# Performance work log

Hardware: AMD Instinct MI355X
Metric: run time of the kernel (lower is better)

## Reference

```python
import jax, jax.numpy as jnp
import numpy as np

THRESH = 0.3
EPS = 1e-8
M = 256
D = 768


def setup_inputs() -> dict:
    key = jax.random.key(0)
    kx, kb, ka, kn = jax.random.split(key, 4)
    x = jax.random.normal(kx, (1, D), dtype=jnp.float32)
    base = jax.random.normal(kb, (M, D), dtype=jnp.float32)
    # correlate memories with x so that a realistic fraction passes the 0.3 cosine threshold
    alpha = jax.random.uniform(ka, (M,), minval=0.0, maxval=0.8)
    mem = alpha[:, None] * x[0][None, :] + jnp.sqrt(1.0 - alpha**2)[:, None] * base
    # pre-sampled injection noise (original: torch.randn * 0.1 per W element)
    noise = 0.1 * jax.random.normal(kn, (M, M, D), dtype=jnp.float32)
    return {"x": x, "mem": mem, "noise": noise}


def reference(x, mem, noise):
    # x: [1, D] query embedding; mem: [M, D] memory bank (k == memory embeddings)
    d = x.shape[-1]
    xv = x[0]                                   # [D]
    nx = jnp.maximum(jnp.linalg.norm(xv), EPS)
    nm = jnp.linalg.norm(mem, axis=-1)          # [M]
    nm_s = jnp.maximum(nm, EPS)
    Sx = xv.sum()
    Sm = mem.sum(-1)                            # [M]

    kx_dot = mem @ xv                           # [M] dot(k_i, x)
    mx_cos = kx_dot / (nm_s * nx)               # [M] cos(x, m_j) == cos(k_i, x)
    mask = (mx_cos > THRESH).astype(x.dtype)    # active memories A
    cnt = mask.sum()

    km_dot = mem @ mem.T                        # [M, M] dot(k_i, m_j)
    km_cos = km_dot / (nm_s[:, None] * nm_s[None, :])

    # c[a, i] = cos(k_i, m_a) + cos(k_i, x)  (scalar added to all D dims of k_i)
    c = km_cos.T + mx_cos[None, :]              # [M, M]

    # ||k'_{a,i}||^2 = ||k_i||^2 + 2 c sum(k_i) + D c^2
    nkp = jnp.sqrt(jnp.maximum(nm[None, :]**2 + 2.0 * c * Sm[None, :] + d * c**2, EPS**2))

    # cos(k'_{a,i}, x) = (dot(k_i,x) + c*sum(x)) / (||k'|| * ||x||)
    cos_kp_x = (kx_dot[None, :] + c * Sx) / (nkp * nx)

    # mean over a' in A of cos(k'_{a,i}, m_{a'}) in closed form
    A1 = (km_dot * (mask / nm_s)[None, :]).sum(-1)   # [M] (i-indexed)
    A2 = ((mask * Sm) / nm_s).sum()                  # scalar
    denom = nkp * jnp.maximum(cnt, 1.0)
    mean_cos_km = jnp.where(cnt > 0, (A1[None, :] + c * A2) / denom, 0.0)

    # W_{a,i} = k'_{a,i} + mean sim to x + mean sim to active mems; then noise; O_prev = 0
    W = mem[None, :, :] + (c + cos_kp_x + mean_cos_km)[:, :, None]   # [M, M, D]
    out = (W + noise) * mask[:, None, None]     # zero rows for inactive memories
    return out
```

## Files before the change

kernel.cpp:

```cpp
#include <hip/hip_runtime.h>
#include <hip/hip_bf16.h>
#include <math.h>

#define M 256
#define D 768
#define D4 (D/4)
#define THRESH 0.3
#define EPS 1e-8

typedef float vfloat4 __attribute__((ext_vector_type(4)));

#define WS_SM    0
#define WS_NM2   256
#define WS_KX    512
#define WS_MASK  768
#define WS_SX    1024
#define WS_NX2   1025
#define WS_MEMT  2048
#define WS_ST    (2048 + D * M)

__global__ __launch_bounds__(256) void k1_stats_transpose(const float* __restrict__ x,
                                                          const float* __restrict__ mem,
                                                          float* __restrict__ ws) {
    const int r = blockIdx.x;
    const int t = threadIdx.x;
    const float* row = (r < M) ? (mem + (size_t)r * D) : x;

    double s = 0.0, sq = 0.0, dt = 0.0;
    for (int d = t; d < D; d += 256) {
        float mf = row[d];
        double m = (double)mf;
        double xv = (double)x[d];
        s += m; sq += m * m; dt += m * xv;
        if (r < M) ws[WS_MEMT + (d >> 2) * (M * 4) + r * 4 + (d & 3)] = mf;
    }
    __shared__ double sh0[256], sh1[256], sh2[256];
    sh0[t] = s; sh1[t] = sq; sh2[t] = dt;
    __syncthreads();
    for (int k = 128; k > 0; k >>= 1) {
        if (t < k) { sh0[t] += sh0[t + k]; sh1[t] += sh1[t + k]; sh2[t] += sh2[t + k]; }
        __syncthreads();
    }
    if (t == 0) {
        if (r < M) {
            ws[WS_SM + r]  = (float)sh0[0];
            ws[WS_NM2 + r] = (float)sh1[0];
            ws[WS_KX + r]  = (float)sh2[0];
        } else {
            ws[WS_SX]  = (float)sh0[0];
            ws[WS_NX2] = (float)sh1[0];
        }
    }
}

__global__ __launch_bounds__(256) void k3_s(const float* __restrict__ mem,
                                            float* __restrict__ ws) {
    const int i = blockIdx.x;
    const int a = threadIdx.x;

    const double nxd   = fmax(sqrt(fmax((double)ws[WS_NX2], 0.0)), EPS);
    const double nm2ad = (double)ws[WS_NM2 + a];
    const double nmsad = fmax(sqrt(fmax(nm2ad, 0.0)), EPS);
    const double mxad  = (double)ws[WS_KX + a] / (nmsad * nxd);
    const float maska = (mxad > THRESH) ? 1.0f : 0.0f;
    const float nmsa  = (float)nmsad;
    if (i == 0) ws[WS_MASK + a] = maska;

    __shared__ vfloat4 lrow4[D4];
    if (a < D4) lrow4[a] = ((const vfloat4*)mem)[(size_t)i * D4 + a];
    __syncthreads();

    const vfloat4* memT4 = (const vfloat4*)(ws + WS_MEMT);
    float acc0 = 0.f, acc1 = 0.f, acc2 = 0.f, acc3 = 0.f;
    for (int dq = 0; dq < D4; dq += 4) {
        vfloat4 v0 = memT4[(dq + 0) * M + a]; vfloat4 l0 = lrow4[dq + 0];
        vfloat4 v1 = memT4[(dq + 1) * M + a]; vfloat4 l1 = lrow4[dq + 1];
        vfloat4 v2 = memT4[(dq + 2) * M + a]; vfloat4 l2 = lrow4[dq + 2];
        vfloat4 v3 = memT4[(dq + 3) * M + a]; vfloat4 l3 = lrow4[dq + 3];
        acc0 += v0.x * l0.x + v0.y * l0.y + v0.z * l0.z + v0.w * l0.w;
        acc1 += v1.x * l1.x + v1.y * l1.y + v1.z * l1.z + v1.w * l1.w;
        acc2 += v2.x * l2.x + v2.y * l2.y + v2.z * l2.z + v2.w * l2.w;
        acc3 += v3.x * l3.x + v3.y * l3.y + v3.z * l3.z + v3.w * l3.w;
    }
    const float g = (acc0 + acc1) + (acc2 + acc3);

    __shared__ float shc[M], sha[M], shr[M];
    shc[a] = maska;
    sha[a] = maska * ws[WS_SM + a] / nmsa;
    shr[a] = (maska / nmsa) * g;
    __syncthreads();
    for (int k = 128; k > 0; k >>= 1) {
        if (a < k) { shc[a] += shc[a + k]; sha[a] += sha[a + k]; shr[a] += shr[a + k]; }
        __syncthreads();
    }
    const float cnt = shc[0];
    const float A2  = sha[0];
    const float A1  = shr[0];

    const float nm2i = ws[WS_NM2 + i];
    const float Smi  = ws[WS_SM + i];
    const float kxi  = ws[WS_KX + i];
    const float nmsi = fmaxf(sqrtf(fmaxf(nm2i, 0.f)), 1e-8f);
    const float nx   = (float)nxd;
    const float Sx   = ws[WS_SX];
    const float mxi  = kxi / (nmsi * nx);

    const float c = g / (nmsa * nmsi) + mxi;
    const float nkp = sqrtf(fmaxf(nm2i + 2.f * c * Smi + (float)D * c * c, 1e-16f));
    const float cos_kp_x = (kxi + c * Sx) / (nkp * nx);
    const float mean_cos_km = (cnt > 0.f) ? (A1 + c * A2) / (nkp * fmaxf(cnt, 1.f)) : 0.f;

    ws[WS_ST + i * M + a] = c + cos_kp_x + mean_cos_km;
}

__global__ __launch_bounds__(D4) void k4_final(const float* __restrict__ mem,
                                               const float* __restrict__ noise,
                                               const float* __restrict__ ws,
                                               float* __restrict__ out) {
    const int a = blockIdx.y;
    const int i0 = blockIdx.x * 16;
    const int t  = threadIdx.x;

    vfloat4* out4 = (vfloat4*)out;
    const size_t base = ((size_t)a * M + i0) * D4 + t;

    if (ws[WS_MASK + a] == 0.0f) {
        const vfloat4 z = (vfloat4){0.f, 0.f, 0.f, 0.f};
        #pragma unroll
        for (int il = 0; il < 16; ++il)
            __builtin_nontemporal_store(z, out4 + base + (size_t)il * D4);
        return;
    }

    const vfloat4* mem4   = (const vfloat4*)mem;
    const vfloat4* noise4 = (const vfloat4*)noise;

    __shared__ float ssh[16];
    if (t < 16) ssh[t] = ws[WS_ST + (i0 + t) * M + a];
    __syncthreads();

    #pragma unroll 4
    for (int il = 0; il < 16; ++il) {
        const float s = ssh[il];
        vfloat4 m = mem4[(size_t)(i0 + il) * D4 + t];
        vfloat4 n = __builtin_nontemporal_load(noise4 + base + (size_t)il * D4);
        vfloat4 o;
        o.x = m.x + s + n.x;
        o.y = m.y + s + n.y;
        o.z = m.z + s + n.z;
        o.w = m.w + s + n.w;
        __builtin_nontemporal_store(o, out4 + base + (size_t)il * D4);
    }
}

extern "C" void kernel_launch(void* const* d_in, const int* in_sizes, int n_in,
                              void* d_out, int out_size, void* d_ws, size_t ws_size,
                              hipStream_t stream) {
    const float* x     = (const float*)d_in[0];
    const float* mem   = (const float*)d_in[1];
    const float* noise = (const float*)d_in[2];
    float* out = (float*)d_out;
    float* ws  = (float*)d_ws;

    k1_stats_transpose<<<dim3(M + 1), dim3(256), 0, stream>>>(x, mem, ws);
    k3_s<<<dim3(M), dim3(256), 0, stream>>>(mem, ws);
    k4_final<<<dim3(16, M), dim3(D4), 0, stream>>>(mem, noise, ws, out);
}
```

Baseline: 339.3 us.

## Fuse three kernels into one cooperative kernel with grid-wide syncs

Replaces the stats/transpose, score and output kernels with a single cooperative launch of 512 blocks that uses grid.sync between phases. The final phase is remapped so each 256-thread block streams 8 groups of 16 rows, with fully unrolled vector loads and stores. The aim is to remove the extra launch gaps and get more in-flight memory traffic in the large noise-to-output stream. In exchange, the work now depends on co-residency of 512 blocks and pays grid-barrier cost, and the big streaming phase runs on a fixed small grid instead of 4096 blocks.

```diff
diff --git a/kernel.cpp b/kernel.cpp
--- a/kernel.cpp
+++ b/kernel.cpp
@@ -1,12 +1,15 @@
 #include <hip/hip_runtime.h>
-#include <hip/hip_bf16.h>
+#include <hip/hip_cooperative_groups.h>
 #include <math.h>
+
+namespace cg = cooperative_groups;
 
 #define M 256
 #define D 768
 #define D4 (D/4)
 #define THRESH 0.3
 #define EPS 1e-8
+#define NBLK 512
 
 typedef float vfloat4 __attribute__((ext_vector_type(4)));
 
@@ -19,137 +22,152 @@
 #define WS_MEMT  2048
 #define WS_ST    (2048 + D * M)
 
-__global__ __launch_bounds__(256) void k1_stats_transpose(const float* __restrict__ x,
-                                                          const float* __restrict__ mem,
-                                                          float* __restrict__ ws) {
-    const int r = blockIdx.x;
+__global__ __launch_bounds__(256, 2) void fused(const float* __restrict__ x,
+                                                const float* __restrict__ mem,
+                                                const float* __restrict__ noise,
+                                                float* __restrict__ ws,
+                                                float* __restrict__ out) {
+    const int b = blockIdx.x;
     const int t = threadIdx.x;
-    const float* row = (r < M) ? (mem + (size_t)r * D) : x;
+    cg::grid_group grid = cg::this_grid();
 
-    double s = 0.0, sq = 0.0, dt = 0.0;
-    for (int d = t; d < D; d += 256) {
-        float mf = row[d];
-        double m = (double)mf;
-        double xv = (double)x[d];
-        s += m; sq += m * m; dt += m * xv;
-        if (r < M) ws[WS_MEMT + (d >> 2) * (M * 4) + r * 4 + (d & 3)] = mf;
-    }
     __shared__ double sh0[256], sh1[256], sh2[256];
-    sh0[t] = s; sh1[t] = sq; sh2[t] = dt;
-    __syncthreads();
-    for (int k = 128; k > 0; k >>= 1) {
-        if (t < k) { sh0[t] += sh0[t + k]; sh1[t] += sh1[t + k]; sh2[t] += sh2[t + k]; }
+    __shared__ vfloat4 lrow4[D4];
+    __shared__ float shc[M], sha[M], shr[M];
+    __shared__ float ssh[8][16];
+    __shared__ float shm[8];
+
+    if (b <= M) {
+        const float* row = (b < M) ? (mem + (size_t)b * D) : x;
+        double s = 0.0, sq = 0.0, dt = 0.0;
+        for (int d = t; d < D; d += 256) {
+            float mf = row[d];
+            double m = (double)mf;
+            double xv = (double)x[d];
+            s += m; sq += m * m; dt += m * xv;
+            if (b < M) ws[WS_MEMT + (d >> 2) * (M * 4) + b * 4 + (d & 3)] = mf;
+        }
+        sh0[t] = s; sh1[t] = sq; sh2[t] = dt;
         __syncthreads();
-    }
-    if (t == 0) {
-        if (r < M) {
-            ws[WS_SM + r]  = (float)sh0[0];
-            ws[WS_NM2 + r] = (float)sh1[0];
-            ws[WS_KX + r]  = (float)sh2[0];
-        } else {
-            ws[WS_SX]  = (float)sh0[0];
-            ws[WS_NX2] = (float)sh1[0];
+        for (int k = 128; k > 0; k >>= 1) {
+            if (t < k) { sh0[t] += sh0[t + k]; sh1[t] += sh1[t + k]; sh2[t] += sh2[t + k]; }
+            __syncthreads();
+        }
+        if (t == 0) {
+            if (b < M) {
+                ws[WS_SM + b]  = (float)sh0[0];
+                ws[WS_NM2 + b] = (float)sh1[0];
+                ws[WS_KX + b]  = (float)sh2[0];
+            } else {
+                ws[WS_SX]  = (float)sh0[0];
+                ws[WS_NX2] = (float)sh1[0];
+            }
         }
     }
-}
+    grid.sync();
 
-__global__ __launch_bounds__(256) void k3_s(const float* __restrict__ mem,
-                                            float* __restrict__ ws) {
-    const int i = blockIdx.x;
-    const int a = threadIdx.x;
+    if (b < M) {
+        const int i = b;
+        const int a = t;
 
-    const double nxd   = fmax(sqrt(fmax((double)ws[WS_NX2], 0.0)), EPS);
-    const double nm2ad = (double)ws[WS_NM2 + a];
-    const double nmsad = fmax(sqrt(fmax(nm2ad, 0.0)), EPS);
-    const double mxad  = (double)ws[WS_KX + a] / (nmsad * nxd);
-    const float maska = (mxad > THRESH) ? 1.0f : 0.0f;
-    const float nmsa  = (float)nmsad;
-    if (i == 0) ws[WS_MASK + a] = maska;
+        const double nxd   = fmax(sqrt(fmax((double)ws[WS_NX2], 0.0)), EPS);
+        const double nm2ad = (double)ws[WS_NM2 + a];
+        const double nmsad = fmax(sqrt(fmax(nm2ad, 0.0)), EPS);
+        const double mxad  = (double)ws[WS_KX + a] / (nmsad * nxd);
+        const float maska = (mxad > THRESH) ? 1.0f : 0.0f;
+        const float nmsa  = (float)nmsad;
+        if (i == 0) ws[WS_MASK + a] = maska;
 
-    __shared__ vfloat4 lrow4[D4];
-    if (a < D4) lrow4[a] = ((const vfloat4*)mem)[(size_t)i * D4 + a];
-    __syncthreads();
+        if (a < D4) lrow4[a] = ((const vfloat4*)mem)[(size_t)i * D4 + a];
+        __syncthreads();
 
-    const vfloat4* memT4 = (const vfloat4*)(ws + WS_MEMT);
-    float acc0 = 0.f, acc1 = 0.f, acc2 = 0.f, acc3 = 0.f;
-    for (int dq = 0; dq < D4; dq += 4) {
-        vfloat4 v0 = memT4[(dq + 0) * M + a]; vfloat4 l0 = lrow4[dq + 0];
-        vfloat4 v1 = memT4[(dq + 1) * M + a]; vfloat4 l1 = lrow4[dq + 1];
-        vfloat4 v2 = memT4[(dq + 2) * M + a]; vfloat4 l2 = lrow4[dq + 2];
-        vfloat4 v3 = memT4[(dq + 3) * M + a]; vfloat4 l3 = lrow4[dq + 3];
-        acc0 += v0.x * l0.x + v0.y * l0.y + v0.z * l0.z + v0.w * l0.w;
-        acc1 += v1.x * l1.x + v1.y * l1.y + v1.z * l1.z + v1.w * l1.w;
-        acc2 += v2.x * l2.x + v2.y * l2.y + v2.z * l2.z + v2.w * l2.w;
-        acc3 += v3.x * l3.x + v3.y * l3.y + v3.z * l3.z + v3.w * l3.w;
+        const vfloat4* memT4 = (const vfloat4*)(ws + WS_MEMT);
+        float acc0 = 0.f, acc1 = 0.f, acc2 = 0.f, acc3 = 0.f;
+        for (int dq = 0; dq < D4; dq += 4) {
+            vfloat4 v0 = memT4[(dq + 0) * M + a]; vfloat4 l0 = lrow4[dq + 0];
+            vfloat4 v1 = memT4[(dq + 1) * M + a]; vfloat4 l1 = lrow4[dq + 1];
+            vfloat4 v2 = memT4[(dq + 2) * M + a]; vfloat4 l2 = lrow4[dq + 2];
+            vfloat4 v3 = memT4[(dq + 3) * M + a]; vfloat4 l3 = lrow4[dq + 3];
+            acc0 += v0.x * l0.x + v0.y * l0.y + v0.z * l0.z + v0.w * l0.w;
+            acc1 += v1.x * l1.x + v1.y * l1.y + v1.z * l1.z + v1.w * l1.w;
+            acc2 += v2.x * l2.x + v2.y * l2.y + v2.z * l2.z + v2.w * l2.w;
+            acc3 += v3.x * l3.x + v3.y * l3.y + v3.z * l3.z + v3.w * l3.w;
+        }
+        const float g = (acc0 + acc1) + (acc2 + acc3);
+
+        shc[a] = maska;
+        sha[a] = maska * ws[WS_SM + a] / nmsa;
+        shr[a] = (maska / nmsa) * g;
+        __syncthreads();
+        for (int k = 128; k > 0; k >>= 1) {
+            if (a < k) { shc[a] += shc[a + k]; sha[a] += sha[a + k]; shr[a] += shr[a + k]; }
+            __syncthreads();
+        }
+        const float cnt = shc[0];
+        const float A2  = sha[0];
+        const float A1  = shr[0];
+
+        const float nm2i = ws[WS_NM2 + i];
+        const float Smi  = ws[WS_SM + i];
+        const float kxi  = ws[WS_KX + i];
+        const float nmsi = fmaxf(sqrtf(fmaxf(nm2i, 0.f)), 1e-8f);
+        const float nx   = (float)nxd;
+        const float Sx   = ws[WS_SX];
+        const float mxi  = kxi / (nmsi * nx);
+
+        const float c = g / (nmsa * nmsi) + mxi;
+        const float nkp = sqrtf(fmaxf(nm2i + 2.f * c * Smi + (float)D * c * c, 1e-16f));
+        const float cos_kp_x = (kxi + c * Sx) / (nkp * nx);
+        const float mean_cos_km = (cnt > 0.f) ? (A1 + c * A2) / (nkp * fmaxf(cnt, 1.f)) : 0.f;
+
+        ws[WS_ST + i * M + a] = c + cos_kp_x + mean_cos_km;
     }
-    const float g = (acc0 + acc1) + (acc2 + acc3);
+    grid.sync();
 
-    __shared__ float shc[M], sha[M], shr[M];
-    shc[a] = maska;
-    sha[a] = maska * ws[WS_SM + a] / nmsa;
-    shr[a] = (maska / nmsa) * g;
-    __syncthreads();
-    for (int k = 128; k > 0; k >>= 1) {
-        if (a < k) { shc[a] += shc[a + k]; sha[a] += sha[a + k]; shr[a] += shr[a + k]; }
+    {
+        const int u0 = b * 8;
+        if (t < 128) {
+            const int j  = t >> 4;
+            const int il = t & 15;
+            const int u  = u0 + j;
+            const int a  = u >> 4;
+            const int i0 = (u & 15) << 4;
+            ssh[j][il] = ws[WS_ST + (i0 + il) * M + a];
+        }
+        if (t < 8) shm[t] = ws[WS_MASK + ((u0 + t) >> 4)];
         __syncthreads();
-    }
-    const float cnt = shc[0];
-    const float A2  = sha[0];
-    const float A1  = shr[0];
 
-    const float nm2i = ws[WS_NM2 + i];
-    const float Smi  = ws[WS_SM + i];
-    const float kxi  = ws[WS_KX + i];
-    const float nmsi = fmaxf(sqrtf(fmaxf(nm2i, 0.f)), 1e-8f);
-    const float nx   = (float)nxd;
-    const float Sx   = ws[WS_SX];
-    const float mxi  = kxi / (nmsi * nx);
+        vfloat4* out4         = (vfloat4*)out;
+        const vfloat4* noise4 = (const vfloat4*)noise;
+        const vfloat4* mem4   = (const vfloat4*)mem;
 
-    const float c = g / (nmsa * nmsi) + mxi;
-    const float nkp = sqrtf(fmaxf(nm2i + 2.f * c * Smi + (float)D * c * c, 1e-16f));
-    const float cos_kp_x = (kxi + c * Sx) / (nkp * nx);
-    const float mean_cos_km = (cnt > 0.f) ? (A1 + c * A2) / (nkp * fmaxf(cnt, 1.f)) : 0.f;
-
-    ws[WS_ST + i * M + a] = c + cos_kp_x + mean_cos_km;
-}
-
-__global__ __launch_bounds__(D4) void k4_final(const float* __restrict__ mem,
-                                               const float* __restrict__ noise,
-                                               const float* __restrict__ ws,
-                                               float* __restrict__ out) {
-    const int a = blockIdx.y;
-    const int i0 = blockIdx.x * 16;
-    const int t  = threadIdx.x;
-
-    vfloat4* out4 = (vfloat4*)out;
-    const size_t base = ((size_t)a * M + i0) * D4 + t;
-
-    if (ws[WS_MASK + a] == 0.0f) {
-        const vfloat4 z = (vfloat4){0.f, 0.f, 0.f, 0.f};
-        #pragma unroll
-        for (int il = 0; il < 16; ++il)
-            __builtin_nontemporal_store(z, out4 + base + (size_t)il * D4);
-        return;
-    }
-
-    const vfloat4* mem4   = (const vfloat4*)mem;
-    const vfloat4* noise4 = (const vfloat4*)noise;
-
-    __shared__ float ssh[16];
-    if (t < 16) ssh[t] = ws[WS_ST + (i0 + t) * M + a];
-    __syncthreads();
-
-    #pragma unroll 4
-    for (int il = 0; il < 16; ++il) {
-        const float s = ssh[il];
-        vfloat4 m = mem4[(size_t)(i0 + il) * D4 + t];
-        vfloat4 n = __builtin_nontemporal_load(noise4 + base + (size_t)il * D4);
-        vfloat4 o;
-        o.x = m.x + s + n.x;
-        o.y = m.y + s + n.y;
-        o.z = m.z + s + n.z;
-        o.w = m.w + s + n.w;
-        __builtin_nontemporal_store(o, out4 + base + (size_t)il * D4);
+        for (int j = 0; j < 8; ++j) {
+            const int u  = u0 + j;
+            const int a  = u >> 4;
+            const int i0 = (u & 15) << 4;
+            const size_t ob = ((size_t)a * M + i0) * D4;
+            if (shm[j] == 0.0f) {
+                const vfloat4 z = (vfloat4){0.f, 0.f, 0.f, 0.f};
+                #pragma unroll
+                for (int k = 0; k < 12; ++k)
+                    __builtin_nontemporal_store(z, out4 + ob + t + k * 256);
+            } else {
+                const size_t mb = (size_t)i0 * D4;
+                #pragma unroll
+                for (int k = 0; k < 12; ++k) {
+                    const int f = t + k * 256;
+                    vfloat4 n = __builtin_nontemporal_load(noise4 + ob + f);
+                    vfloat4 m = mem4[mb + f];
+                    const float s = ssh[j][f / 192];
+                    vfloat4 o;
+                    o.x = m.x + s + n.x;
+                    o.y = m.y + s + n.y;
+                    o.z = m.z + s + n.z;
+                    o.w = m.w + s + n.w;
+                    __builtin_nontemporal_store(o, out4 + ob + f);
+                }
+            }
+        }
     }
 }
 
@@ -162,7 +180,6 @@
     float* out = (float*)d_out;
     float* ws  = (float*)d_ws;
 
-    k1_stats_transpose<<<dim3(M + 1), dim3(256), 0, stream>>>(x, mem, ws);
-    k3_s<<<dim3(M), dim3(256), 0, stream>>>(mem, ws);
-    k4_final<<<dim3(16, M), dim3(D4), 0, stream>>>(mem, noise, ws, out);
+    void* args[] = {(void*)&x, (void*)&mem, (void*)&noise, (void*)&ws, (void*)&out};
+    hipLaunchCooperativeKernel((void*)fused, dim3(NBLK), dim3(256), args, 0, stream);
 }
```

Result: slower. 456.5 us (+34.5%).

## Merge stats and similarity kernels into one cooperative kernel with grid sync

Applied to the files above, without the earlier changes.

Fuses the row-statistics/transpose kernel and the similarity-scalar kernel into a single cooperative launch separated by a grid-wide sync, removing one kernel launch boundary. Block size doubles to 512 so two half-blocks split the D dimension of the Gram dot product and combine through shared memory. The noise load in the final kernel switches from a nontemporal load to a regular load. Cooperative launch adds grid.sync overhead and requires all 256 blocks to be co-resident.

```diff
diff --git a/kernel.cpp b/kernel.cpp
--- a/kernel.cpp
+++ b/kernel.cpp
@@ -1,6 +1,8 @@
 #include <hip/hip_runtime.h>
-#include <hip/hip_bf16.h>
+#include <hip/hip_cooperative_groups.h>
 #include <math.h>
+
+namespace cg = cooperative_groups;
 
 #define M 256
 #define D 768
@@ -19,105 +21,132 @@
 #define WS_MEMT  2048
 #define WS_ST    (2048 + D * M)
 
-__global__ __launch_bounds__(256) void k1_stats_transpose(const float* __restrict__ x,
-                                                          const float* __restrict__ mem,
-                                                          float* __restrict__ ws) {
-    const int r = blockIdx.x;
+__global__ __launch_bounds__(512) void kA(const float* __restrict__ x,
+                                          const float* __restrict__ mem,
+                                          float* __restrict__ ws) {
+    const int b = blockIdx.x;
     const int t = threadIdx.x;
-    const float* row = (r < M) ? (mem + (size_t)r * D) : x;
+    cg::grid_group grid = cg::this_grid();
 
-    double s = 0.0, sq = 0.0, dt = 0.0;
-    for (int d = t; d < D; d += 256) {
-        float mf = row[d];
-        double m = (double)mf;
-        double xv = (double)x[d];
-        s += m; sq += m * m; dt += m * xv;
-        if (r < M) ws[WS_MEMT + (d >> 2) * (M * 4) + r * 4 + (d & 3)] = mf;
+    __shared__ double sh0[512], sh1[512], sh2[512];
+
+    {
+        const float* row = mem + (size_t)b * D;
+        double s = 0.0, sq = 0.0, dt = 0.0;
+        for (int d = t; d < D; d += 512) {
+            float mf = row[d];
+            double m = (double)mf;
+            double xv = (double)x[d];
+            s += m; sq += m * m; dt += m * xv;
+            ws[WS_MEMT + (d >> 2) * (M * 4) + b * 4 + (d & 3)] = mf;
+        }
+        sh0[t] = s; sh1[t] = sq; sh2[t] = dt;
+        __syncthreads();
+        for (int k = 256; k > 0; k >>= 1) {
+            if (t < k) { sh0[t] += sh0[t + k]; sh1[t] += sh1[t + k]; sh2[t] += sh2[t + k]; }
+            __syncthreads();
+        }
+        if (t == 0) {
+            ws[WS_SM + b]  = (float)sh0[0];
+            ws[WS_NM2 + b] = (float)sh1[0];
+            ws[WS_KX + b]  = (float)sh2[0];
+        }
+        if (b == 0) {
+            __syncthreads();
+            double s2 = 0.0, sq2 = 0.0;
+            for (int d = t; d < D; d += 512) {
+                double xv = (double)x[d];
+                s2 += xv; sq2 += xv * xv;
+            }
+            sh0[t] = s2; sh1[t] = sq2;
+            __syncthreads();
+            for (int k = 256; k > 0; k >>= 1) {
+                if (t < k) { sh0[t] += sh0[t + k]; sh1[t] += sh1[t + k]; }
+                __syncthreads();
+            }
+            if (t == 0) {
+                ws[WS_SX]  = (float)sh0[0];
+                ws[WS_NX2] = (float)sh1[0];
+            }
+        }
     }
-    __shared__ double sh0[256], sh1[256], sh2[256];
-    sh0[t] = s; sh1[t] = sq; sh2[t] = dt;
-    __syncthreads();
-    for (int k = 128; k > 0; k >>= 1) {
-        if (t < k) { sh0[t] += sh0[t + k]; sh1[t] += sh1[t + k]; sh2[t] += sh2[t + k]; }
+    grid.sync();
+
+    {
+        const int i = b;
+        const int a = t & 255;
+        const int h = t >> 8;
+
+        const double nxd   = fmax(sqrt(fmax((double)ws[WS_NX2], 0.0)), EPS);
+        const double nm2ad = (double)ws[WS_NM2 + a];
+        const double nmsad = fmax(sqrt(fmax(nm2ad, 0.0)), EPS);
+        const double mxad  = (double)ws[WS_KX + a] / (nmsad * nxd);
+        const float maska = (mxad > THRESH) ? 1.0f : 0.0f;
+        const float nmsa  = (float)nmsad;
+        if (i == 0 && h == 0) ws[WS_MASK + a] = maska;
+
+        __shared__ vfloat4 lrow4[D4];
+        if (t < D4) lrow4[t] = ((const vfloat4*)mem)[(size_t)i * D4 + t];
         __syncthreads();
-    }
-    if (t == 0) {
-        if (r < M) {
-            ws[WS_SM + r]  = (float)sh0[0];
-            ws[WS_NM2 + r] = (float)sh1[0];
-            ws[WS_KX + r]  = (float)sh2[0];
-        } else {
-            ws[WS_SX]  = (float)sh0[0];
-            ws[WS_NX2] = (float)sh1[0];
+
+        const vfloat4* memT4 = (const vfloat4*)(ws + WS_MEMT);
+        float acc0 = 0.f, acc1 = 0.f, acc2 = 0.f, acc3 = 0.f;
+        const int dq0 = h * 96;
+        for (int dq = dq0; dq < dq0 + 96; dq += 4) {
+            vfloat4 v0 = memT4[(dq + 0) * M + a]; vfloat4 l0 = lrow4[dq + 0];
+            vfloat4 v1 = memT4[(dq + 1) * M + a]; vfloat4 l1 = lrow4[dq + 1];
+            vfloat4 v2 = memT4[(dq + 2) * M + a]; vfloat4 l2 = lrow4[dq + 2];
+            vfloat4 v3 = memT4[(dq + 3) * M + a]; vfloat4 l3 = lrow4[dq + 3];
+            acc0 += v0.x * l0.x + v0.y * l0.y + v0.z * l0.z + v0.w * l0.w;
+            acc1 += v1.x * l1.x + v1.y * l1.y + v1.z * l1.z + v1.w * l1.w;
+            acc2 += v2.x * l2.x + v2.y * l2.y + v2.z * l2.z + v2.w * l2.w;
+            acc3 += v3.x * l3.x + v3.y * l3.y + v3.z * l3.z + v3.w * l3.w;
+        }
+        __shared__ float shg[512];
+        shg[t] = (acc0 + acc1) + (acc2 + acc3);
+        __syncthreads();
+        const float g = shg[a] + shg[a + 256];
+
+        __shared__ float shc[M], sha[M], shr[M];
+        if (h == 0) {
+            shc[a] = maska;
+            sha[a] = maska * ws[WS_SM + a] / nmsa;
+            shr[a] = (maska / nmsa) * g;
+        }
+        __syncthreads();
+        for (int k = 128; k > 0; k >>= 1) {
+            if (t < k) { shc[t] += shc[t + k]; sha[t] += sha[t + k]; shr[t] += shr[t + k]; }
+            __syncthreads();
+        }
+
+        if (h == 0) {
+            const float cnt = shc[0];
+            const float A2  = sha[0];
+            const float A1  = shr[0];
+
+            const float nm2i = ws[WS_NM2 + i];
+            const float Smi  = ws[WS_SM + i];
+            const float kxi  = ws[WS_KX + i];
+            const float nmsi = fmaxf(sqrtf(fmaxf(nm2i, 0.f)), 1e-8f);
+            const float nx   = (float)nxd;
+            const float Sx   = ws[WS_SX];
+            const float mxi  = kxi / (nmsi * nx);
+
+            const float c = g / (nmsa * nmsi) + mxi;
+            const float nkp = sqrtf(fmaxf(nm2i + 2.f * c * Smi + (float)D * c * c, 1e-16f));
+            const float cos_kp_x = (kxi + c * Sx) / (nkp * nx);
+            const float mean_cos_km = (cnt > 0.f) ? (A1 + c * A2) / (nkp * fmaxf(cnt, 1.f)) : 0.f;
+
+            ws[WS_ST + i * M + a] = c + cos_kp_x + mean_cos_km;
         }
     }
 }
 
-__global__ __launch_bounds__(256) void k3_s(const float* __restrict__ mem,
-                                            float* __restrict__ ws) {
-    const int i = blockIdx.x;
-    const int a = threadIdx.x;
-
-    const double nxd   = fmax(sqrt(fmax((double)ws[WS_NX2], 0.0)), EPS);
-    const double nm2ad = (double)ws[WS_NM2 + a];
-    const double nmsad = fmax(sqrt(fmax(nm2ad, 0.0)), EPS);
-    const double mxad  = (double)ws[WS_KX + a] / (nmsad * nxd);
-    const float maska = (mxad > THRESH) ? 1.0f : 0.0f;
-    const float nmsa  = (float)nmsad;
-    if (i == 0) ws[WS_MASK + a] = maska;
-
-    __shared__ vfloat4 lrow4[D4];
-    if (a < D4) lrow4[a] = ((const vfloat4*)mem)[(size_t)i * D4 + a];
-    __syncthreads();
-
-    const vfloat4* memT4 = (const vfloat4*)(ws + WS_MEMT);
-    float acc0 = 0.f, acc1 = 0.f, acc2 = 0.f, acc3 = 0.f;
-    for (int dq = 0; dq < D4; dq += 4) {
-        vfloat4 v0 = memT4[(dq + 0) * M + a]; vfloat4 l0 = lrow4[dq + 0];
-        vfloat4 v1 = memT4[(dq + 1) * M + a]; vfloat4 l1 = lrow4[dq + 1];
-        vfloat4 v2 = memT4[(dq + 2) * M + a]; vfloat4 l2 = lrow4[dq + 2];
-        vfloat4 v3 = memT4[(dq + 3) * M + a]; vfloat4 l3 = lrow4[dq + 3];
-        acc0 += v0.x * l0.x + v0.y * l0.y + v0.z * l0.z + v0.w * l0.w;
-        acc1 += v1.x * l1.x + v1.y * l1.y + v1.z * l1.z + v1.w * l1.w;
-        acc2 += v2.x * l2.x + v2.y * l2.y + v2.z * l2.z + v2.w * l2.w;
-        acc3 += v3.x * l3.x + v3.y * l3.y + v3.z * l3.z + v3.w * l3.w;
-    }
-    const float g = (acc0 + acc1) + (acc2 + acc3);
-
-    __shared__ float shc[M], sha[M], shr[M];
-    shc[a] = maska;
-    sha[a] = maska * ws[WS_SM + a] / nmsa;
-    shr[a] = (maska / nmsa) * g;
-    __syncthreads();
-    for (int k = 128; k > 0; k >>= 1) {
-        if (a < k) { shc[a] += shc[a + k]; sha[a] += sha[a + k]; shr[a] += shr[a + k]; }
-        __syncthreads();
-    }
-    const float cnt = shc[0];
-    const float A2  = sha[0];
-    const float A1  = shr[0];
-
-    const float nm2i = ws[WS_NM2 + i];
-    const float Smi  = ws[WS_SM + i];
-    const float kxi  = ws[WS_KX + i];
-    const float nmsi = fmaxf(sqrtf(fmaxf(nm2i, 0.f)), 1e-8f);
-    const float nx   = (float)nxd;
-    const float Sx   = ws[WS_SX];
-    const float mxi  = kxi / (nmsi * nx);
-
-    const float c = g / (nmsa * nmsi) + mxi;
-    const float nkp = sqrtf(fmaxf(nm2i + 2.f * c * Smi + (float)D * c * c, 1e-16f));
-    const float cos_kp_x = (kxi + c * Sx) / (nkp * nx);
-    const float mean_cos_km = (cnt > 0.f) ? (A1 + c * A2) / (nkp * fmaxf(cnt, 1.f)) : 0.f;
-
-    ws[WS_ST + i * M + a] = c + cos_kp_x + mean_cos_km;
-}
-
-__global__ __launch_bounds__(D4) void k4_final(const float* __restrict__ mem,
-                                               const float* __restrict__ noise,
-                                               const float* __restrict__ ws,
-                                               float* __restrict__ out) {
-    const int a = blockIdx.y;
+__global__ __launch_bounds__(D4) void kB(const float* __restrict__ mem,
+                                         const float* __restrict__ noise,
+                                         const float* __restrict__ ws,
+                                         float* __restrict__ out) {
+    const int a  = blockIdx.y;
     const int i0 = blockIdx.x * 16;
     const int t  = threadIdx.x;
 
@@ -143,7 +172,7 @@
     for (int il = 0; il < 16; ++il) {
         const float s = ssh[il];
         vfloat4 m = mem4[(size_t)(i0 + il) * D4 + t];
-        vfloat4 n = __builtin_nontemporal_load(noise4 + base + (size_t)il * D4);
+        vfloat4 n = noise4[base + (size_t)il * D4];
         vfloat4 o;
         o.x = m.x + s + n.x;
         o.y = m.y + s + n.y;
@@ -162,7 +191,7 @@
     float* out = (float*)d_out;
     float* ws  = (float*)d_ws;
 
-    k1_stats_transpose<<<dim3(M + 1), dim3(256), 0, stream>>>(x, mem, ws);
-    k3_s<<<dim3(M), dim3(256), 0, stream>>>(mem, ws);
-    k4_final<<<dim3(16, M), dim3(D4), 0, stream>>>(mem, noise, ws, out);
+    void* argsA[] = {(void*)&x, (void*)&mem, (void*)&ws};
+    hipLaunchCooperativeKernel((void*)kA, dim3(M), dim3(512), argsA, 0, stream);
+    kB<<<dim3(16, M), dim3(D4), 0, stream>>>(mem, noise, ws, out);
 }
```

New measurement: 380.1 us. 1.12x slower.

## Move zero-fill of inactive rows into gram kernel and compute mask earlier

Applied to the files above, without the earlier changes.

The per-row mask is now computed in the stats kernel, which lets the gram kernel also launch extra blocks that zero-fill output rows for inactive memories, running alongside the gram computation. The final streaming kernel then exits early for inactive rows and only handles the active ones. The nontemporal hint on the noise load is dropped for a plain load. Each stats block now redundantly reduces x sums. This adds 4096 extra blocks to the gram launch in exchange for a lighter final kernel.

```diff
diff --git a/kernel.cpp b/kernel.cpp
--- a/kernel.cpp
+++ b/kernel.cpp
@@ -1,5 +1,4 @@
 #include <hip/hip_runtime.h>
-#include <hip/hip_bf16.h>
 #include <math.h>
 
 #define M 256
@@ -7,6 +6,7 @@
 #define D4 (D/4)
 #define THRESH 0.3
 #define EPS 1e-8
+#define ZFB 4096
 
 typedef float vfloat4 __attribute__((ext_vector_type(4)));
 
@@ -19,52 +19,75 @@
 #define WS_MEMT  2048
 #define WS_ST    (2048 + D * M)
 
-__global__ __launch_bounds__(256) void k1_stats_transpose(const float* __restrict__ x,
-                                                          const float* __restrict__ mem,
-                                                          float* __restrict__ ws) {
+__global__ __launch_bounds__(256) void k1_stats(const float* __restrict__ x,
+                                                const float* __restrict__ mem,
+                                                float* __restrict__ ws) {
     const int r = blockIdx.x;
     const int t = threadIdx.x;
-    const float* row = (r < M) ? (mem + (size_t)r * D) : x;
+    const float* row = mem + (size_t)r * D;
 
-    double s = 0.0, sq = 0.0, dt = 0.0;
+    double s = 0.0, sq = 0.0, dt = 0.0, xs = 0.0, xq = 0.0;
     for (int d = t; d < D; d += 256) {
         float mf = row[d];
-        double m = (double)mf;
+        double m  = (double)mf;
         double xv = (double)x[d];
         s += m; sq += m * m; dt += m * xv;
-        if (r < M) ws[WS_MEMT + (d >> 2) * (M * 4) + r * 4 + (d & 3)] = mf;
+        xs += xv; xq += xv * xv;
+        ws[WS_MEMT + (d >> 2) * (M * 4) + r * 4 + (d & 3)] = mf;
     }
-    __shared__ double sh0[256], sh1[256], sh2[256];
-    sh0[t] = s; sh1[t] = sq; sh2[t] = dt;
+    __shared__ double sh0[256], sh1[256], sh2[256], sh3[256], sh4[256];
+    sh0[t] = s; sh1[t] = sq; sh2[t] = dt; sh3[t] = xs; sh4[t] = xq;
     __syncthreads();
     for (int k = 128; k > 0; k >>= 1) {
-        if (t < k) { sh0[t] += sh0[t + k]; sh1[t] += sh1[t + k]; sh2[t] += sh2[t + k]; }
+        if (t < k) {
+            sh0[t] += sh0[t + k]; sh1[t] += sh1[t + k]; sh2[t] += sh2[t + k];
+            sh3[t] += sh3[t + k]; sh4[t] += sh4[t + k];
+        }
         __syncthreads();
     }
     if (t == 0) {
-        if (r < M) {
-            ws[WS_SM + r]  = (float)sh0[0];
-            ws[WS_NM2 + r] = (float)sh1[0];
-            ws[WS_KX + r]  = (float)sh2[0];
-        } else {
-            ws[WS_SX]  = (float)sh0[0];
-            ws[WS_NX2] = (float)sh1[0];
-        }
+        const float smf  = (float)sh0[0];
+        const float nm2f = (float)sh1[0];
+        const float kxf  = (float)sh2[0];
+        const float sxf  = (float)sh3[0];
+        const float nx2f = (float)sh4[0];
+        ws[WS_SM + r]  = smf;
+        ws[WS_NM2 + r] = nm2f;
+        ws[WS_KX + r]  = kxf;
+        if (r == 0) { ws[WS_SX] = sxf; ws[WS_NX2] = nx2f; }
+        const double nxd  = fmax(sqrt(fmax((double)nx2f, 0.0)), EPS);
+        const double nmsd = fmax(sqrt(fmax((double)nm2f, 0.0)), EPS);
+        const double mxd  = (double)kxf / (nmsd * nxd);
+        ws[WS_MASK + r] = (mxd > THRESH) ? 1.0f : 0.0f;
     }
 }
 
-__global__ __launch_bounds__(256) void k3_s(const float* __restrict__ mem,
-                                            float* __restrict__ ws) {
-    const int i = blockIdx.x;
-    const int a = threadIdx.x;
+__global__ __launch_bounds__(256) void k2_gram_zfill(const float* __restrict__ mem,
+                                                     float* __restrict__ ws,
+                                                     float* __restrict__ out) {
+    const int bid = blockIdx.x;
+    const int t   = threadIdx.x;
 
-    const double nxd   = fmax(sqrt(fmax((double)ws[WS_NX2], 0.0)), EPS);
-    const double nm2ad = (double)ws[WS_NM2 + a];
-    const double nmsad = fmax(sqrt(fmax(nm2ad, 0.0)), EPS);
-    const double mxad  = (double)ws[WS_KX + a] / (nmsad * nxd);
-    const float maska = (mxad > THRESH) ? 1.0f : 0.0f;
-    const float nmsa  = (float)nmsad;
-    if (i == 0) ws[WS_MASK + a] = maska;
+    if (bid >= M) {
+        const int u = bid - M;
+        const int a = u >> 4;
+        if (ws[WS_MASK + a] != 0.0f) return;
+        const int i0 = (u & 15) << 4;
+        vfloat4* out4 = (vfloat4*)out;
+        const size_t base = ((size_t)a * M + i0) * D4;
+        const vfloat4 z = (vfloat4){0.f, 0.f, 0.f, 0.f};
+        #pragma unroll
+        for (int k = 0; k < 12; ++k)
+            __builtin_nontemporal_store(z, out4 + base + t + k * 256);
+        return;
+    }
+
+    const int i = bid;
+    const int a = t;
+
+    const float maska = ws[WS_MASK + a];
+    const double nmsad = fmax(sqrt(fmax((double)ws[WS_NM2 + a], 0.0)), EPS);
+    const float  nmsa  = (float)nmsad;
 
     __shared__ vfloat4 lrow4[D4];
     if (a < D4) lrow4[a] = ((const vfloat4*)mem)[(size_t)i * D4 + a];
@@ -101,7 +124,7 @@
     const float Smi  = ws[WS_SM + i];
     const float kxi  = ws[WS_KX + i];
     const float nmsi = fmaxf(sqrtf(fmaxf(nm2i, 0.f)), 1e-8f);
-    const float nx   = (float)nxd;
+    const float nx   = fmaxf(sqrtf(fmaxf(ws[WS_NX2], 0.f)), 1e-8f);
     const float Sx   = ws[WS_SX];
     const float mxi  = kxi / (nmsi * nx);
 
@@ -113,27 +136,19 @@
     ws[WS_ST + i * M + a] = c + cos_kp_x + mean_cos_km;
 }
 
-__global__ __launch_bounds__(D4) void k4_final(const float* __restrict__ mem,
-                                               const float* __restrict__ noise,
-                                               const float* __restrict__ ws,
-                                               float* __restrict__ out) {
+__global__ __launch_bounds__(D4) void k3_stream(const float* __restrict__ mem,
+                                                const float* __restrict__ noise,
+                                                const float* __restrict__ ws,
+                                                float* __restrict__ out) {
     const int a = blockIdx.y;
+    if (ws[WS_MASK + a] == 0.0f) return;
     const int i0 = blockIdx.x * 16;
     const int t  = threadIdx.x;
 
-    vfloat4* out4 = (vfloat4*)out;
-    const size_t base = ((size_t)a * M + i0) * D4 + t;
-
-    if (ws[WS_MASK + a] == 0.0f) {
-        const vfloat4 z = (vfloat4){0.f, 0.f, 0.f, 0.f};
-        #pragma unroll
-        for (int il = 0; il < 16; ++il)
-            __builtin_nontemporal_store(z, out4 + base + (size_t)il * D4);
-        return;
-    }
-
     const vfloat4* mem4   = (const vfloat4*)mem;
     const vfloat4* noise4 = (const vfloat4*)noise;
+    vfloat4* out4         = (vfloat4*)out;
+    const size_t base = ((size_t)a * M + i0) * D4 + t;
 
     __shared__ float ssh[16];
     if (t < 16) ssh[t] = ws[WS_ST + (i0 + t) * M + a];
@@ -143,7 +158,7 @@
     for (int il = 0; il < 16; ++il) {
         const float s = ssh[il];
         vfloat4 m = mem4[(size_t)(i0 + il) * D4 + t];
-        vfloat4 n = __builtin_nontemporal_load(noise4 + base + (size_t)il * D4);
+        vfloat4 n = noise4[base + (size_t)il * D4];
         vfloat4 o;
         o.x = m.x + s + n.x;
         o.y = m.y + s + n.y;
@@ -162,7 +177,7 @@
     float* out = (float*)d_out;
     float* ws  = (float*)d_ws;
 
-    k1_stats_transpose<<<dim3(M + 1), dim3(256), 0, stream>>>(x, mem, ws);
-    k3_s<<<dim3(M), dim3(256), 0, stream>>>(mem, ws);
-    k4_final<<<dim3(16, M), dim3(D4), 0, stream>>>(mem, noise, ws, out);
+    k1_stats<<<dim3(M), dim3(256), 0, stream>>>(x, mem, ws);
+    k2_gram_zfill<<<dim3(M + ZFB), dim3(256), 0, stream>>>(mem, ws, out);
+    k3_stream<<<dim3(16, M), dim3(D4), 0, stream>>>(mem, noise, ws, out);
 }
```

Result: no change. 335.1 us (-1.2%).
